# Optimization experiments

Measured on AMD Instinct MI355X. Metric: run time of the kernel, lower is better.

Reference implementation:

```python
import jax, jax.numpy as jnp
import numpy as np


def setup_inputs() -> dict:
    key = jax.random.key(0)
    k1, k2, k3, k4 = jax.random.split(key, 4)
    T, D, N = 8192, 128, 32
    x = jax.random.normal(k1, (T, D), dtype=jnp.float32)
    h_a0 = jax.random.normal(k2, (N, D), dtype=jnp.float32)
    h_sd0 = jax.random.uniform(k3, (N, D), dtype=jnp.float32)
    alpha = jax.random.uniform(k4, (N, D), dtype=jnp.float32)  # nn.Parameter uniform(0,1)
    return {"x": x, "h_a0": h_a0, "h_sd0": h_sd0, "alpha": alpha}


def reference(x, h_a0, h_sd0, alpha):
    # EMA with standard deviation (with_SD=True), expressed as a lax.scan
    # over the time axis. h state: (h_a, h_v) each (num_N, input_dim).
    h_v0 = h_sd0 ** 2

    def step(carry, x_i):
        h_a, h_v = carry
        d = x_i[None, :] - h_a            # (N, D)
        h_v = (1.0 - alpha) * (h_v + alpha * d * d)
        h_a = h_a + alpha * d
        return (h_a, h_v), (h_a, h_v)

    (hN_a, hN_v), (out_a, out_v) = jax.lax.scan(step, (h_a0, h_v0), x)
    # out_a/out_v: (T, N, D); torch code concatenates avg and sqrt(var) on dim 1
    out = jnp.concatenate([out_a, jnp.sqrt(out_v)], axis=1)  # (T, 2N, D)
    return out, hN_a, jnp.sqrt(hN_v)
```

## Files before the change

kernel.cpp:

```cpp
#include <hip/hip_runtime.h>
#include <math.h>

typedef float vf4 __attribute__((ext_vector_type(4)));

constexpr int T = 8192;
constexpr int D = 128;
constexpr int N = 32;
constexpr int L = 64;
constexpr int LOG2L = 6;
constexpr int K = T / L;
constexpr int S = N * D;
constexpr int S4 = S / 4;
constexpr int D4 = D / 4;
constexpr int OSTRIDE4 = (2 * N * D) / 4;

__device__ __forceinline__ float fast_sqrt(float x) {
    float r;
    asm("v_sqrt_f32 %0, %1" : "=v"(r) : "v"(x));
    return r;
}

__global__ __launch_bounds__(256) void k1_summaries(
    const vf4* __restrict__ x, const vf4* __restrict__ alpha,
    vf4* __restrict__ c_a, vf4* __restrict__ cA, vf4* __restrict__ cP)
{
    int gid = blockIdx.x * 256 + threadIdx.x;
    int k   = gid >> 10;
    int s4  = gid & (S4 - 1);
    int d4  = s4 & (D4 - 1);

    vf4 a = alpha[s4];
    vf4 b = 1.0f - a;
    vf4 q = {0.f, 0.f, 0.f, 0.f};
    vf4 A = {0.f, 0.f, 0.f, 0.f};
    vf4 P = {0.f, 0.f, 0.f, 0.f};
    const vf4* xp = x + (size_t)k * L * D4 + d4;
#pragma unroll 8
    for (int i = 0; i < L; ++i) {
        vf4 xv = xp[(size_t)i * D4];
        vf4 p  = xv - q;
        P += p;
        A = b * (A + (a * p) * p);
        q = q + a * p;
    }
    c_a[gid] = q;
    cA[gid]  = A;
    cP[gid]  = P;
}

__global__ __launch_bounds__(64) void k2_scan(
    const vf4* __restrict__ h_a0, const vf4* __restrict__ h_sd0,
    const vf4* __restrict__ alpha,
    const vf4* __restrict__ c_a, const vf4* __restrict__ cA,
    const vf4* __restrict__ cP,
    vf4* __restrict__ h_a_start, vf4* __restrict__ h_v_start,
    float* __restrict__ out)
{
    int s4 = blockIdx.x * 64 + threadIdx.x;
    vf4 a = alpha[s4];
    vf4 b = 1.0f - a;
    vf4 bl = b;
#pragma unroll
    for (int i = 0; i < LOG2L; ++i) bl *= bl;
    vf4 Cq = bl * (1.0f - bl);
    vf4 Bc = a * bl;

    vf4 ha = h_a0[s4];
    vf4 sd = h_sd0[s4];
    vf4 hv = sd * sd;
#pragma unroll 8
    for (int k = 0; k < K; ++k) {
        size_t idx = (size_t)k * S4 + s4;
        vf4 ca = c_a[idx];
        vf4 Ak = cA[idx];
        vf4 Pk = cP[idx];
        h_a_start[idx] = ha;
        vf4 hvc;
#pragma unroll
        for (int j = 0; j < 4; ++j) hvc[j] = fmaxf(hv[j], 0.f);
        h_v_start[idx] = hvc;
        vf4 cv = Ak - 2.0f * ((Bc * Pk) * ha) + Cq * (ha * ha);
        ha = bl * ha + ca;
        hv = bl * hvc + cv;
    }
    vf4* tail = (vf4*)(out + (size_t)T * 2 * N * D);
    tail[s4] = ha;
    vf4 r;
#pragma unroll
    for (int j = 0; j < 4; ++j) r[j] = fast_sqrt(fmaxf(hv[j], 0.f));
    tail[S4 + s4] = r;
}

__global__ __launch_bounds__(256) void k3_fused(
    const vf4* __restrict__ x, const vf4* __restrict__ alpha,
    const vf4* __restrict__ h_a_start, const vf4* __restrict__ h_v_start,
    vf4* __restrict__ out)
{
    int gid = blockIdx.x * 256 + threadIdx.x;
    int k   = gid >> 10;
    int s4  = gid & (S4 - 1);
    int n   = s4 >> 5;
    int d4  = s4 & (D4 - 1);

    vf4 a = alpha[s4];
    vf4 b = 1.0f - a;
    vf4 h = h_a_start[gid];
    vf4 v = h_v_start[gid];
    const vf4* xp = x + (size_t)k * L * D4 + d4;
    vf4* opa = out + (size_t)k * L * OSTRIDE4 + n * D4 + d4;
    vf4* opv = opa + N * D4;
#pragma unroll 8
    for (int i = 0; i < L; ++i) {
        vf4 xv  = xp[(size_t)i * D4];
        vf4 dx  = xv - h;
        vf4 adx = a * dx;
        v = b * (v + adx * dx);
        h = h + adx;
        vf4 r;
#pragma unroll
        for (int j = 0; j < 4; ++j) r[j] = fast_sqrt(v[j]);
        opa[(size_t)i * OSTRIDE4] = h;
        opv[(size_t)i * OSTRIDE4] = r;
    }
}

extern "C" void kernel_launch(void* const* d_in, const int* in_sizes, int n_in,
                              void* d_out, int out_size, void* d_ws, size_t ws_size,
                              hipStream_t stream) {
    const vf4* x     = (const vf4*)d_in[0];
    const vf4* h_a0  = (const vf4*)d_in[1];
    const vf4* h_sd0 = (const vf4*)d_in[2];
    const vf4* alpha = (const vf4*)d_in[3];
    float* out = (float*)d_out;
    float* ws  = (float*)d_ws;

    vf4* c_a       = (vf4*)(ws + 0 * (size_t)K * S);
    vf4* cA        = (vf4*)(ws + 1 * (size_t)K * S);
    vf4* cP        = (vf4*)(ws + 2 * (size_t)K * S);
    vf4* h_a_start = (vf4*)(ws + 3 * (size_t)K * S);
    vf4* h_v_start = (vf4*)(ws + 4 * (size_t)K * S);

    dim3 big(K * S4 / 256);
    dim3 blk(256);

    k1_summaries<<<big, blk, 0, stream>>>(x, alpha, c_a, cA, cP);
    k2_scan<<<dim3(S4 / 64), dim3(64), 0, stream>>>(h_a0, h_sd0, alpha,
                                                    c_a, cA, cP,
                                                    h_a_start, h_v_start, out);
    k3_fused<<<big, blk, 0, stream>>>(x, alpha, h_a_start, h_v_start, (vf4*)out);
}
```

Before: 351.3 us.

## Parallelize chunk scan across segments with shared-memory carry aggregation

Halves the chunk length and splits the sequential middle scan into 8 segments per column. Each segment computes local aggregates, combines the carries of earlier segments through shared memory, then re-scans its own chunks. The workspace buffers are reused in place to store chunk start states, and the final kernel writes its output with nontemporal stores. The goal is to remove the long serial dependency chain in the middle kernel, which previously ran only 16 blocks of 64 threads. In exchange it adds extra passes over the workspace and more chunk summaries, which raises memory traffic in the first and last kernels.

```diff
diff --git a/kernel.cpp b/kernel.cpp
--- a/kernel.cpp
+++ b/kernel.cpp
@@ -6,13 +6,17 @@
 constexpr int T = 8192;
 constexpr int D = 128;
 constexpr int N = 32;
-constexpr int L = 64;
-constexpr int LOG2L = 6;
+constexpr int L = 32;
+constexpr int LOG2L = 5;
 constexpr int K = T / L;
 constexpr int S = N * D;
 constexpr int S4 = S / 4;
 constexpr int D4 = D / 4;
 constexpr int OSTRIDE4 = (2 * N * D) / 4;
+
+constexpr int SEG  = 8;
+constexpr int CPS  = K / SEG;
+constexpr int COLS = 32;
 
 __device__ __forceinline__ float fast_sqrt(float x) {
     float r;
@@ -48,47 +52,89 @@
     cP[gid]  = P;
 }
 
-__global__ __launch_bounds__(64) void k2_scan(
+__global__ __launch_bounds__(256) void k2_scan(
     const vf4* __restrict__ h_a0, const vf4* __restrict__ h_sd0,
     const vf4* __restrict__ alpha,
-    const vf4* __restrict__ c_a, const vf4* __restrict__ cA,
-    const vf4* __restrict__ cP,
-    vf4* __restrict__ h_a_start, vf4* __restrict__ h_v_start,
+    vf4* __restrict__ buf0,
+    vf4* __restrict__ buf1,
+    const vf4* __restrict__ buf2,
     float* __restrict__ out)
 {
-    int s4 = blockIdx.x * 64 + threadIdx.x;
+    __shared__ vf4 Cagg[SEG][COLS];
+    __shared__ vf4 Vagg[SEG][COLS];
+
+    int t   = threadIdx.x;
+    int col = t & (COLS - 1);
+    int kg  = t >> 5;
+    int s4  = blockIdx.x * COLS + col;
+    int kbase = kg * CPS;
+
     vf4 a = alpha[s4];
     vf4 b = 1.0f - a;
     vf4 bl = b;
 #pragma unroll
     for (int i = 0; i < LOG2L; ++i) bl *= bl;
+    vf4 M = bl;
+#pragma unroll
+    for (int i = 0; i < 5; ++i) M *= M;
     vf4 Cq = bl * (1.0f - bl);
     vf4 Bc = a * bl;
 
-    vf4 ha = h_a0[s4];
+    vf4 C = {0.f, 0.f, 0.f, 0.f};
+#pragma unroll 4
+    for (int j = 0; j < CPS; ++j) {
+        vf4 ca = buf0[(size_t)(kbase + j) * S4 + s4];
+        C = bl * C + ca;
+    }
+    Cagg[kg][col] = C;
+    __syncthreads();
+
+    vf4 H = h_a0[s4];
+    for (int g = 0; g < kg; ++g) H = M * H + Cagg[g][col];
+
+    vf4 Vg = {0.f, 0.f, 0.f, 0.f};
+#pragma unroll 4
+    for (int j = 0; j < CPS; ++j) {
+        size_t idx = (size_t)(kbase + j) * S4 + s4;
+        vf4 ca = buf0[idx];
+        vf4 Ak = buf1[idx];
+        vf4 Pk = buf2[idx];
+        buf0[idx] = H;
+        vf4 cv = Ak - 2.0f * ((Bc * Pk) * H) + Cq * (H * H);
+        Vg = bl * Vg + cv;
+        H  = bl * H + ca;
+    }
+    Vagg[kg][col] = Vg;
+    if (kg == SEG - 1) {
+        vf4* tail = (vf4*)(out + (size_t)T * 2 * N * D);
+        tail[s4] = H;
+    }
+    __syncthreads();
+
     vf4 sd = h_sd0[s4];
-    vf4 hv = sd * sd;
-#pragma unroll 8
-    for (int k = 0; k < K; ++k) {
-        size_t idx = (size_t)k * S4 + s4;
-        vf4 ca = c_a[idx];
-        vf4 Ak = cA[idx];
-        vf4 Pk = cP[idx];
-        h_a_start[idx] = ha;
-        vf4 hvc;
+    vf4 V = sd * sd;
+    for (int g = 0; g < kg; ++g) V = M * V + Vagg[g][col];
+
+#pragma unroll 4
+    for (int j = 0; j < CPS; ++j) {
+        size_t idx = (size_t)(kbase + j) * S4 + s4;
+        vf4 Hk = buf0[idx];
+        vf4 Ak = buf1[idx];
+        vf4 Pk = buf2[idx];
+        vf4 Vc;
 #pragma unroll
-        for (int j = 0; j < 4; ++j) hvc[j] = fmaxf(hv[j], 0.f);
-        h_v_start[idx] = hvc;
-        vf4 cv = Ak - 2.0f * ((Bc * Pk) * ha) + Cq * (ha * ha);
-        ha = bl * ha + ca;
-        hv = bl * hvc + cv;
+        for (int jj = 0; jj < 4; ++jj) Vc[jj] = fmaxf(V[jj], 0.f);
+        buf1[idx] = Vc;
+        vf4 cv = Ak - 2.0f * ((Bc * Pk) * Hk) + Cq * (Hk * Hk);
+        V = bl * Vc + cv;
     }
-    vf4* tail = (vf4*)(out + (size_t)T * 2 * N * D);
-    tail[s4] = ha;
-    vf4 r;
+    if (kg == SEG - 1) {
+        vf4* tail = (vf4*)(out + (size_t)T * 2 * N * D);
+        vf4 r;
 #pragma unroll
-    for (int j = 0; j < 4; ++j) r[j] = fast_sqrt(fmaxf(hv[j], 0.f));
-    tail[S4 + s4] = r;
+        for (int jj = 0; jj < 4; ++jj) r[jj] = fast_sqrt(fmaxf(V[jj], 0.f));
+        tail[S4 + s4] = r;
+    }
 }
 
 __global__ __launch_bounds__(256) void k3_fused(
@@ -119,8 +165,8 @@
         vf4 r;
 #pragma unroll
         for (int j = 0; j < 4; ++j) r[j] = fast_sqrt(v[j]);
-        opa[(size_t)i * OSTRIDE4] = h;
-        opv[(size_t)i * OSTRIDE4] = r;
+        __builtin_nontemporal_store(h, &opa[(size_t)i * OSTRIDE4]);
+        __builtin_nontemporal_store(r, &opv[(size_t)i * OSTRIDE4]);
     }
 }
 
@@ -134,18 +180,15 @@
     float* out = (float*)d_out;
     float* ws  = (float*)d_ws;
 
-    vf4* c_a       = (vf4*)(ws + 0 * (size_t)K * S);
-    vf4* cA        = (vf4*)(ws + 1 * (size_t)K * S);
-    vf4* cP        = (vf4*)(ws + 2 * (size_t)K * S);
-    vf4* h_a_start = (vf4*)(ws + 3 * (size_t)K * S);
-    vf4* h_v_start = (vf4*)(ws + 4 * (size_t)K * S);
+    vf4* buf0 = (vf4*)(ws + 0 * (size_t)K * S);
+    vf4* buf1 = (vf4*)(ws + 1 * (size_t)K * S);
+    vf4* buf2 = (vf4*)(ws + 2 * (size_t)K * S);
 
     dim3 big(K * S4 / 256);
     dim3 blk(256);
 
-    k1_summaries<<<big, blk, 0, stream>>>(x, alpha, c_a, cA, cP);
-    k2_scan<<<dim3(S4 / 64), dim3(64), 0, stream>>>(h_a0, h_sd0, alpha,
-                                                    c_a, cA, cP,
-                                                    h_a_start, h_v_start, out);
-    k3_fused<<<big, blk, 0, stream>>>(x, alpha, h_a_start, h_v_start, (vf4*)out);
+    k1_summaries<<<big, blk, 0, stream>>>(x, alpha, buf0, buf1, buf2);
+    k2_scan<<<dim3(S4 / COLS), blk, 0, stream>>>(h_a0, h_sd0, alpha,
+                                                 buf0, buf1, buf2, out);
+    k3_fused<<<big, blk, 0, stream>>>(x, alpha, buf0, buf1, (vf4*)out);
 }
```

Result: faster. 293.5 us (-16.5%).
